# Optimization experiments

Hardware: AMD Instinct MI355X
Metric: run time of the kernel (lower is better)

## Reference

```python
import jax, jax.numpy as jnp
import numpy as np

B, C, CI, H, W = 4, 64, 32, 96, 96  # batch, in_channels, inter_channels, height, width


def conv2d(x, w, b, stride=1, pad=0):
    out = jax.lax.conv_general_dilated(
        x, w, (stride, stride), [(pad, pad), (pad, pad)],
        dimension_numbers=('NCHW', 'OIHW', 'NCHW'))
    return out + b[None, :, None, None]


def maxpool2(x):
    return jax.lax.reduce_window(x, -jnp.inf, jax.lax.max, (1, 1, 2, 2), (1, 1, 2, 2), 'VALID')


def up2(x):
    return jnp.repeat(jnp.repeat(x, 2, axis=2), 2, axis=3)


def bn_train(x, gamma, beta, eps=1e-5):
    # BatchNorm2d in training mode: batch statistics over (N, H, W)
    m = jnp.mean(x, axis=(0, 2, 3), keepdims=True)
    v = jnp.var(x, axis=(0, 2, 3), keepdims=True)
    return gamma[None, :, None, None] * (x - m) * jax.lax.rsqrt(v + eps) + beta[None, :, None, None]


def setup_inputs() -> dict:
    key = jax.random.key(0)
    ks = jax.random.split(key, 20)
    s1 = (2.0 / C) ** 0.5            # kaiming-ish for 1x1 convs
    s3 = (2.0 / (C * 9)) ** 0.5      # kaiming-ish for 3x3 convs
    sw = (2.0 / CI) ** 0.5
    return {
        'x':         jax.random.normal(ks[0], (B, C, H, W), jnp.float32),
        'x_pan':     jax.random.normal(ks[1], (B, C, H, W), jnp.float32),
        'g_w':       jax.random.normal(ks[2], (CI, C, 1, 1), jnp.float32) * s1,
        'g_b':       jnp.zeros((CI,), jnp.float32),
        'g_pan_w':   jax.random.normal(ks[3], (CI, C, 1, 1), jnp.float32) * s1,
        'g_pan_b':   jnp.zeros((CI,), jnp.float32),
        'theta_w':   jax.random.normal(ks[4], (CI, C, 3, 3), jnp.float32) * s3,
        'theta_b':   jax.random.normal(ks[5], (CI,), jnp.float32) * 0.02,
        'phi_w':     jax.random.normal(ks[6], (CI, C, 3, 3), jnp.float32) * s3,
        'phi_b':     jax.random.normal(ks[7], (CI,), jnp.float32) * 0.02,
        'phi_pan_w': jax.random.normal(ks[8], (CI, C, 3, 3), jnp.float32) * s3,
        'phi_pan_b': jax.random.normal(ks[9], (CI,), jnp.float32) * 0.02,
        'W_w':       jax.random.normal(ks[10], (C, CI, 1, 1), jnp.float32) * sw,
        'W_b':       jnp.zeros((C,), jnp.float32),
        'W_gamma':   jnp.ones((C,), jnp.float32),
        'W_beta':    jnp.zeros((C,), jnp.float32),
        'Wp_w':      jax.random.normal(ks[11], (C, CI, 1, 1), jnp.float32) * sw,
        'Wp_b':      jnp.zeros((C,), jnp.float32),
        'Wp_gamma':  jnp.ones((C,), jnp.float32),
        'Wp_beta':   jnp.zeros((C,), jnp.float32),
    }


def reference(x, x_pan, g_w, g_b, g_pan_w, g_pan_b, theta_w, theta_b,
              phi_w, phi_b, phi_pan_w, phi_pan_b,
              W_w, W_b, W_gamma, W_beta, Wp_w, Wp_b, Wp_gamma, Wp_beta):
    b = x.shape[0]
    # self branch
    g_x = maxpool2(conv2d(x, g_w, g_b)).reshape(b, CI, -1)                           # (B,CI,M)
    theta = up2(conv2d(x, theta_w, theta_b, stride=2, pad=1)).reshape(b, CI, -1)     # (B,CI,N)
    phi = up2(maxpool2(conv2d(x, phi_w, phi_b, stride=2, pad=1))).reshape(b, CI, -1) # (B,CI,M)
    f = jnp.einsum('bcn,bcm->bnm', theta, phi)                                       # (B,N,M)
    a = jax.nn.softmax(f, axis=-1)
    y = jnp.einsum('bnm,bcm->bcn', a, g_x).reshape(b, CI, H, W)
    W_y = bn_train(conv2d(y, W_w, W_b), W_gamma, W_beta)
    # cross-modal (pan) branch, sharing theta queries
    g_p = maxpool2(conv2d(x_pan, g_pan_w, g_pan_b)).reshape(b, CI, -1)
    phi_p = up2(maxpool2(conv2d(x_pan, phi_pan_w, phi_pan_b, stride=2, pad=1))).reshape(b, CI, -1)
    f_p = jnp.einsum('bcn,bcm->bnm', theta, phi_p)
    a_p = jax.nn.softmax(f_p, axis=-1)
    y_p = jnp.einsum('bnm,bcm->bcn', a_p, g_p).reshape(b, CI, H, W)
    Wp_y = bn_train(conv2d(y_p, Wp_w, Wp_b), Wp_gamma, Wp_beta)
    return jnp.concatenate([W_y, Wp_y], axis=1)  # (B, 2C, H, W)
```

## Files before the change

kernel.cpp:

```cpp
#include <hip/hip_runtime.h>
#include <math.h>

#define BB   4
#define CIN  64
#define CMID 32
#define HS   96
#define WS   96
#define H2   48
#define W2   48
#define H4   24
#define W4   24
#define N2   (H2*W2)
#define M4   (H4*W4)

__global__ __launch_bounds__(128) void conv3x3_kernel(
    const float* __restrict__ x, const float* __restrict__ x_pan,
    const float* __restrict__ theta_w, const float* __restrict__ phi_w,
    const float* __restrict__ phi_pan_w,
    float* __restrict__ Ptheta, float* __restrict__ Pphi)
{
    const int bx = blockIdx.x;
    const int b  = blockIdx.y;
    const int cz = blockIdx.z;

    __shared__ __align__(16) float xs[8][5][104];
    __shared__ float wsm[8][9][32];

    const int tid = threadIdx.x;
    const int c16 = tid & 15;
    const int g   = tid >> 4;

    const float* xin = (cz == 2) ? x_pan : x;
    const float* wgt = (cz == 0) ? theta_w : (cz == 1 ? phi_w : phi_pan_w);

    const int p    = bx >> 1;
    const int half = bx & 1;
    const int row0 = 4*p - 1;

    float acc[2][2][6];
    #pragma unroll
    for (int u = 0; u < 2; ++u)
        #pragma unroll
        for (int o = 0; o < 2; ++o)
            #pragma unroll
            for (int j = 0; j < 6; ++j) acc[u][o][j] = 0.f;

    for (int chunk = 0; chunk < 4; ++chunk) {
        const int ci0 = half*32 + chunk*8;
        __syncthreads();
        for (int u = tid; u < 8*5*26; u += 128) {
            int ci = u / 130, rem = u % 130, rr = rem / 26, k = rem % 26;
            int row = row0 + rr;
            float4 v = {0.f,0.f,0.f,0.f};
            if (row >= 0 && row < HS && k >= 2)
                v = *(const float4*)&xin[((b*CIN + ci0 + ci)*HS + row)*WS + 4*k - 8];
            *(float4*)&xs[ci][rr][4*k] = v;
        }
        for (int u = tid; u < 576; u += 128) {
            int c2 = u / 18, f = u % 18;
            float4 wv = *(const float4*)&wgt[c2*576 + ci0*9 + 4*f];
            int lin = 4*f;
            wsm[(lin  )/9][(lin  )%9][c2] = wv.x;
            wsm[(lin+1)/9][(lin+1)%9][c2] = wv.y;
            wsm[(lin+2)/9][(lin+2)%9][c2] = wv.z;
            wsm[(lin+3)/9][(lin+3)%9][c2] = wv.w;
        }
        __syncthreads();

        for (int ci = 0; ci < 8; ++ci) {
            float w9a[9], w9b[9];
            #pragma unroll
            for (int kk = 0; kk < 9; ++kk) {
                w9a[kk] = wsm[ci][kk][c16];
                w9b[kk] = wsm[ci][kk][c16 + 16];
            }
            #pragma unroll
            for (int rr = 0; rr < 5; ++rr) {
                const float4* xr = (const float4*)&xs[ci][rr][12*g + 4];
                float4 t0 = xr[0], t1 = xr[1], t2 = xr[2], t3 = xr[3];
                float xv[16] = {t0.x,t0.y,t0.z,t0.w, t1.x,t1.y,t1.z,t1.w,
                                t2.x,t2.y,t2.z,t2.w, t3.x,t3.y,t3.z,t3.w};
                if (rr <= 2) {
                    #pragma unroll
                    for (int j = 0; j < 6; ++j)
                        #pragma unroll
                        for (int kw = 0; kw < 3; ++kw) {
                            float xvv = xv[3 + 2*j + kw];
                            acc[0][0][j] += w9a[rr*3+kw] * xvv;
                            acc[1][0][j] += w9b[rr*3+kw] * xvv;
                        }
                }
                if (rr >= 2) {
                    #pragma unroll
                    for (int j = 0; j < 6; ++j)
                        #pragma unroll
                        for (int kw = 0; kw < 3; ++kw) {
                            float xvv = xv[3 + 2*j + kw];
                            acc[0][1][j] += w9a[(rr-2)*3+kw] * xvv;
                            acc[1][1][j] += w9b[(rr-2)*3+kw] * xvv;
                        }
                }
            }
        }
    }

    if (cz == 0) {
        #pragma unroll
        for (int u = 0; u < 2; ++u)
            #pragma unroll
            for (int o = 0; o < 2; ++o)
                #pragma unroll
                for (int j = 0; j < 6; ++j) {
                    int n = (2*p + o)*48 + 6*g + j;
                    Ptheta[((size_t)(half*4 + b)*N2 + n)*32 + c16 + 16*u] = acc[u][o][j];
                }
    } else {
        const int brn = cz - 1;
        #pragma unroll
        for (int u = 0; u < 2; ++u) {
            float* Pb = Pphi + (size_t)(((half*2 + brn)*4 + b)*32 + c16 + 16*u)*N2;
            #pragma unroll
            for (int o = 0; o < 2; ++o)
                #pragma unroll
                for (int j = 0; j < 6; ++j)
                    Pb[(2*p + o)*48 + 6*g + j] = acc[u][o][j];
        }
    }
}

__global__ __launch_bounds__(256) void phipool_kernel(
    const float* __restrict__ Pphi,
    const float* __restrict__ phi_b, const float* __restrict__ phi_pan_b,
    float* __restrict__ Kp)
{
    const int o = blockIdx.x*256 + threadIdx.x;
    const int br   = o / 73728;
    const int rem  = o % 73728;
    const int b    = rem / 18432;
    const int rem2 = rem % 18432;
    const int co   = rem2 / 576;
    const int k    = rem2 % 576;
    const int pr   = k / 24, pc = k % 24;

    const int h1 = 2*4*32*N2;
    const int base = (((br*4 + b)*32 + co)*48 + 2*pr)*48 + 2*pc;
    float2 a0 = *(const float2*)&Pphi[base];
    float2 a1 = *(const float2*)&Pphi[base + 48];
    float2 c0 = *(const float2*)&Pphi[h1 + base];
    float2 c1 = *(const float2*)&Pphi[h1 + base + 48];
    float v00 = a0.x + c0.x, v01 = a0.y + c0.y;
    float v10 = a1.x + c1.x, v11 = a1.y + c1.y;
    float bv = (br ? phi_pan_b : phi_b)[co];
    Kp[((size_t)(br*4 + b)*576 + k)*32 + co] =
        fmaxf(fmaxf(v00, v01), fmaxf(v10, v11)) + bv;
}

__global__ __launch_bounds__(384) void gconv_kernel(
    const float* __restrict__ x, const float* __restrict__ x_pan,
    const float* __restrict__ g_w, const float* __restrict__ g_b,
    const float* __restrict__ g_pan_w, const float* __restrict__ g_pan_b,
    float* __restrict__ Vt)
{
    const int r4 = blockIdx.x;
    const int ch = blockIdx.y;
    const int bb = blockIdx.z;
    const int br = bb >> 2, b = bb & 3;
    const float* xin = br ? x_pan : x;
    const float* wg  = br ? g_pan_w : g_w;

    __shared__ __align__(16) float xs[32][4][48];
    __shared__ float wl[64*33];
    const int tid = threadIdx.x;
    for (int u = tid; u < 2048; u += 384) {
        int c2 = u >> 6, ci = u & 63;
        wl[ci*33 + c2] = wg[u];
    }

    const int c  = tid & 31;
    const int sl = tid >> 5;
    float4 ac0 = {0,0,0,0}, ac1 = {0,0,0,0}, ac2 = {0,0,0,0}, ac3 = {0,0,0,0};

    for (int ci0 = 0; ci0 < 64; ci0 += 32) {
        __syncthreads();
        for (int u = tid; u < 32*4*12; u += 384) {
            int ci = u / 48, rem = u % 48, r = rem / 12, k = rem % 12;
            *(float4*)&xs[ci][r][4*k] =
                *(const float4*)&xin[((b*64 + ci0 + ci)*96 + 4*r4 + r)*96 + ch*48 + 4*k];
        }
        __syncthreads();
        for (int ci = 0; ci < 32; ++ci) {
            const float wv = wl[(ci0 + ci)*33 + c];
            float4 x0 = *(const float4*)&xs[ci][0][4*sl];
            float4 x1 = *(const float4*)&xs[ci][1][4*sl];
            float4 x2 = *(const float4*)&xs[ci][2][4*sl];
            float4 x3 = *(const float4*)&xs[ci][3][4*sl];
            ac0.x += wv*x0.x; ac0.y += wv*x0.y; ac0.z += wv*x0.z; ac0.w += wv*x0.w;
            ac1.x += wv*x1.x; ac1.y += wv*x1.y; ac1.z += wv*x1.z; ac1.w += wv*x1.w;
            ac2.x += wv*x2.x; ac2.y += wv*x2.y; ac2.z += wv*x2.z; ac2.w += wv*x2.w;
            ac3.x += wv*x3.x; ac3.y += wv*x3.y; ac3.z += wv*x3.z; ac3.w += wv*x3.w;
        }
    }
    float m00 = fmaxf(fmaxf(ac0.x, ac0.y), fmaxf(ac1.x, ac1.y));
    float m01 = fmaxf(fmaxf(ac0.z, ac0.w), fmaxf(ac1.z, ac1.w));
    float m10 = fmaxf(fmaxf(ac2.x, ac2.y), fmaxf(ac3.x, ac3.y));
    float m11 = fmaxf(fmaxf(ac2.z, ac2.w), fmaxf(ac3.z, ac3.w));
    float bv = (br ? g_pan_b : g_b)[c];
    const int k = r4*24 + ch*12 + sl;
    Vt[((size_t)bb*32 + c)*576 + k] = 0.25f*(m00+m01+m10+m11) + bv;
}

__global__ __launch_bounds__(576, 5) void attn_kernel(
    const float* __restrict__ Ptheta, const float* __restrict__ theta_b,
    const float* __restrict__ Kp, const float* __restrict__ Vt,
    const float* __restrict__ W_w, const float* __restrict__ W_b,
    const float* __restrict__ Wp_w, const float* __restrict__ Wp_b,
    float* __restrict__ zbuf, float* __restrict__ Pp1, float* __restrict__ Pp2)
{
    const int qt = blockIdx.x;
    const int bb = blockIdx.y;
    const int b  = bb & 3;
    const int br = bb >> 2;
    const int q0 = qt*16;

    __shared__ __align__(16) float Pt[16*580];
    __shared__ __align__(16) float Qs[16*36];
    __shared__ float ybuf[16*36];
    __shared__ float Wt[32*64];
    __shared__ float zinv[16];
    __shared__ float s1b[512], s2b[512];

    const int tid = threadIdx.x;

    if (tid < 512) {
        const int q = tid >> 5, c = tid & 31;
        Qs[q*36 + c] = Ptheta[((size_t)b*N2 + q0 + q)*32 + c]
                     + Ptheta[((size_t)(4 + b)*N2 + q0 + q)*32 + c]
                     + theta_b[c];
    }
    const float* Wsrc = br ? Wp_w : W_w;
    for (int u = tid; u < 2048; u += 576) {
        const int o = u >> 5, c = u & 31;
        Wt[c*64 + o] = Wsrc[u];
    }
    __syncthreads();

    {
        const float* krow = Kp + ((size_t)bb*576 + tid)*32;
        float4 kf[8];
        #pragma unroll
        for (int i = 0; i < 8; ++i) kf[i] = ((const float4*)krow)[i];
        float s[16];
        #pragma unroll
        for (int q = 0; q < 16; ++q) {
            const float4* qr = (const float4*)&Qs[q*36];
            float a0 = 0.f, a1 = 0.f, a2 = 0.f, a3 = 0.f;
            #pragma unroll
            for (int i = 0; i < 8; ++i) {
                float4 qf = qr[i];
                a0 += qf.x*kf[i].x; a1 += qf.y*kf[i].y;
                a2 += qf.z*kf[i].z; a3 += qf.w*kf[i].w;
            }
            s[q] = (a0 + a1) + (a2 + a3);
        }
        #pragma unroll
        for (int q = 0; q < 16; ++q) Pt[q*580 + tid] = s[q];
    }
    __syncthreads();

    if (tid < 256) {
        const int q = tid >> 4, sl = tid & 15;
        float* row = &Pt[q*580 + 36*sl];
        float4 f[9];
        #pragma unroll
        for (int j = 0; j < 9; ++j) f[j] = *(const float4*)&row[4*j];
        float m = -1e30f;
        #pragma unroll
        for (int j = 0; j < 9; ++j)
            m = fmaxf(m, fmaxf(fmaxf(f[j].x, f[j].y), fmaxf(f[j].z, f[j].w)));
        m = fmaxf(m, __shfl_xor(m, 1));
        m = fmaxf(m, __shfl_xor(m, 2));
        m = fmaxf(m, __shfl_xor(m, 4));
        m = fmaxf(m, __shfl_xor(m, 8));
        float z = 0.f;
        #pragma unroll
        for (int j = 0; j < 9; ++j) {
            f[j].x = __expf(f[j].x - m); f[j].y = __expf(f[j].y - m);
            f[j].z = __expf(f[j].z - m); f[j].w = __expf(f[j].w - m);
            z += (f[j].x + f[j].y) + (f[j].z + f[j].w);
            *(float4*)&row[4*j] = f[j];
        }
        z += __shfl_xor(z, 1); z += __shfl_xor(z, 2);
        z += __shfl_xor(z, 4); z += __shfl_xor(z, 8);
        if (sl == 0) zinv[q] = 1.0f / z;
    }
    __syncthreads();

    if (tid < 512) {
        const int q = tid >> 5, c = tid & 31;
        const float* vrow = Vt + ((size_t)bb*32 + c)*576;
        const float* prow = &Pt[q*580];
        float a0 = 0.f, a1 = 0.f, a2 = 0.f, a3 = 0.f;
        #pragma unroll 4
        for (int kk = 0; kk < 144; ++kk) {
            float4 pa = *(const float4*)&prow[4*kk];
            float4 va = *(const float4*)&vrow[4*kk];
            a0 += pa.x*va.x; a1 += pa.y*va.y;
            a2 += pa.z*va.z; a3 += pa.w*va.w;
        }
        ybuf[q*36 + c] = ((a0 + a1) + (a2 + a3)) * zinv[q];
    }
    __syncthreads();

    if (tid < 512) {
        const int q = tid >> 5, o2 = tid & 31;
        const float* Wbias = br ? Wp_b : W_b;
        float z0a = 0.f, z0b = 0.f, z1a = 0.f, z1b = 0.f;
        #pragma unroll
        for (int c2 = 0; c2 < 32; c2 += 2) {
            float y0 = ybuf[q*36 + c2], y1 = ybuf[q*36 + c2 + 1];
            z0a += Wt[c2*64 + o2]*y0;        z0b += Wt[(c2+1)*64 + o2]*y1;
            z1a += Wt[c2*64 + o2 + 32]*y0;   z1b += Wt[(c2+1)*64 + o2 + 32]*y1;
        }
        float z0 = Wbias[o2]      + z0a + z0b;
        float z1 = Wbias[o2 + 32] + z1a + z1b;
        const int n = q0 + q;
        zbuf[((size_t)(br*64 + o2)*4 + b)*N2 + n]      = z0;
        zbuf[((size_t)(br*64 + o2 + 32)*4 + b)*N2 + n] = z1;
        float t0 = z0 + __shfl_xor(z0, 32);
        float t1 = z1 + __shfl_xor(z1, 32);
        float u0 = z0*z0; u0 += __shfl_xor(u0, 32);
        float u1 = z1*z1; u1 += __shfl_xor(u1, 32);
        if ((tid & 32) == 0) {
            const int w = tid >> 6;
            s1b[w*64 + o2]      = t0;  s1b[w*64 + o2 + 32] = t1;
            s2b[w*64 + o2]      = u0;  s2b[w*64 + o2 + 32] = u1;
        }
    }
    __syncthreads();
    if (tid < 64) {
        float ps = 0.f, pq = 0.f;
        #pragma unroll
        for (int w = 0; w < 8; ++w) { ps += s1b[w*64 + tid]; pq += s2b[w*64 + tid]; }
        Pp1[(size_t)(br*64 + tid)*576 + b*144 + qt] = ps;
        Pp2[(size_t)(br*64 + tid)*576 + b*144 + qt] = pq;
    }
}

__global__ __launch_bounds__(576) void bnup_kernel(
    const float* __restrict__ zbuf,
    const float* __restrict__ Pp1, const float* __restrict__ Pp2,
    const float* __restrict__ W_gamma, const float* __restrict__ W_beta,
    const float* __restrict__ Wp_gamma, const float* __restrict__ Wp_beta,
    float* __restrict__ out)
{
    const int og = blockIdx.x, b = blockIdx.y;
    const int br = og >> 6, o = og & 63;
    const int t = threadIdx.x;

    __shared__ float sb1[9], sb2[9], bc[2];
    float ps = Pp1[(size_t)og*576 + t];
    float pq = Pp2[(size_t)og*576 + t];
    #pragma unroll
    for (int d = 1; d < 64; d <<= 1) {
        ps += __shfl_xor(ps, d);
        pq += __shfl_xor(pq, d);
    }
    if ((t & 63) == 0) { sb1[t >> 6] = ps; sb2[t >> 6] = pq; }
    __syncthreads();
    if (t == 0) {
        float s = 0.f, qq = 0.f;
        #pragma unroll
        for (int w = 0; w < 9; ++w) { s += sb1[w]; qq += sb2[w]; }
        const float mean = s * (1.0f/9216.0f);
        const float var  = qq * (1.0f/9216.0f) - mean*mean;
        const float gamma = (br ? Wp_gamma : W_gamma)[o];
        const float beta  = (br ? Wp_beta  : W_beta)[o];
        const float scale = gamma * rsqrtf(var + 1e-5f);
        bc[0] = scale; bc[1] = beta - mean*scale;
    }
    __syncthreads();
    const float scale = bc[0], shift = bc[1];

    float4 a = *(const float4*)&zbuf[((size_t)og*4 + b)*N2 + 4*t];
    const int r = t / 12, cs = t % 12;
    float v0 = a.x*scale + shift, v1 = a.y*scale + shift;
    float v2 = a.z*scale + shift, v3 = a.w*scale + shift;
    float4 lo = {v0, v0, v1, v1};
    float4 hi = {v2, v2, v3, v3};
    float* ob = out + ((size_t)(b*128 + og)*96 + 2*r)*96 + 8*cs;
    *(float4*)(ob)       = lo;
    *(float4*)(ob + 4)   = hi;
    *(float4*)(ob + 96)  = lo;
    *(float4*)(ob + 100) = hi;
}

extern "C" void kernel_launch(void* const* d_in, const int* in_sizes, int n_in,
                              void* d_out, int out_size, void* d_ws, size_t ws_size,
                              hipStream_t stream) {
    (void)in_sizes; (void)n_in; (void)out_size; (void)ws_size;
    const float* x         = (const float*)d_in[0];
    const float* x_pan     = (const float*)d_in[1];
    const float* g_w       = (const float*)d_in[2];
    const float* g_b       = (const float*)d_in[3];
    const float* g_pan_w   = (const float*)d_in[4];
    const float* g_pan_b   = (const float*)d_in[5];
    const float* theta_w   = (const float*)d_in[6];
    const float* theta_b   = (const float*)d_in[7];
    const float* phi_w     = (const float*)d_in[8];
    const float* phi_b     = (const float*)d_in[9];
    const float* phi_pan_w = (const float*)d_in[10];
    const float* phi_pan_b = (const float*)d_in[11];
    const float* W_w       = (const float*)d_in[12];
    const float* W_b       = (const float*)d_in[13];
    const float* W_gamma   = (const float*)d_in[14];
    const float* W_beta    = (const float*)d_in[15];
    const float* Wp_w      = (const float*)d_in[16];
    const float* Wp_b      = (const float*)d_in[17];
    const float* Wp_gamma  = (const float*)d_in[18];
    const float* Wp_beta   = (const float*)d_in[19];

    float* out = (float*)d_out;
    float* ws  = (float*)d_ws;

    float* Ptheta = ws;
    float* Pphi   = Ptheta + 589824;
    float* zbuf   = Pphi;
    float* Kp     = Pphi + 1179648;
    float* Vt     = Kp + 147456;
    float* Pp1    = Vt + 147456;
    float* Pp2    = Pp1 + 73728;

    conv3x3_kernel<<<dim3(48, 4, 3), 128, 0, stream>>>(
        x, x_pan, theta_w, phi_w, phi_pan_w, Ptheta, Pphi);
    phipool_kernel<<<dim3(576), 256, 0, stream>>>(Pphi, phi_b, phi_pan_b, Kp);
    gconv_kernel<<<dim3(24, 2, 8), 384, 0, stream>>>(
        x, x_pan, g_w, g_b, g_pan_w, g_pan_b, Vt);
    attn_kernel<<<dim3(144, 8), 576, 0, stream>>>(
        Ptheta, theta_b, Kp, Vt, W_w, W_b, Wp_w, Wp_b, zbuf, Pp1, Pp2);
    bnup_kernel<<<dim3(128, 4), 576, 0, stream>>>(
        zbuf, Pp1, Pp2, W_gamma, W_beta, Wp_gamma, Wp_beta, out);
}
```

Baseline: 444.6 us.

## Split conv3x3 output rows across more threads and stage V tiles in shared memory

The 3x3 conv kernel doubles its block to 256 threads. Each thread half now computes one output row instead of two, and each staging chunk loads 16 input channels instead of 8. The attention kernel drops the occupancy hint from its launch bounds, pads the score rows differently, and stages Vt in 144-column chunks in shared memory for the P·V product instead of streaming it from global memory per thread. The goals are more parallelism in the conv and coalesced, reused V loads in attention, at the cost of more shared memory and extra barriers.

```diff
diff --git a/kernel.cpp b/kernel.cpp
--- a/kernel.cpp
+++ b/kernel.cpp
@@ -13,7 +13,7 @@
 #define N2   (H2*W2)
 #define M4   (H4*W4)
 
-__global__ __launch_bounds__(128) void conv3x3_kernel(
+__global__ __launch_bounds__(256) void conv3x3_kernel(
     const float* __restrict__ x, const float* __restrict__ x_pan,
     const float* __restrict__ theta_w, const float* __restrict__ phi_w,
     const float* __restrict__ phi_pan_w,
@@ -23,12 +23,13 @@
     const int b  = blockIdx.y;
     const int cz = blockIdx.z;
 
-    __shared__ __align__(16) float xs[8][5][104];
-    __shared__ float wsm[8][9][32];
+    __shared__ __align__(16) float xs[16][5][104];
+    __shared__ float wsm[16][9][32];
 
     const int tid = threadIdx.x;
     const int c16 = tid & 15;
-    const int g   = tid >> 4;
+    const int g   = (tid >> 4) & 7;
+    const int r   = tid >> 7;
 
     const float* xin = (cz == 2) ? x_pan : x;
     const float* wgt = (cz == 0) ? theta_w : (cz == 1 ? phi_w : phi_pan_w);
@@ -37,18 +38,16 @@
     const int half = bx & 1;
     const int row0 = 4*p - 1;
 
-    float acc[2][2][6];
+    float acc[2][6];
     #pragma unroll
     for (int u = 0; u < 2; ++u)
         #pragma unroll
-        for (int o = 0; o < 2; ++o)
-            #pragma unroll
-            for (int j = 0; j < 6; ++j) acc[u][o][j] = 0.f;
-
-    for (int chunk = 0; chunk < 4; ++chunk) {
-        const int ci0 = half*32 + chunk*8;
-        __syncthreads();
-        for (int u = tid; u < 8*5*26; u += 128) {
+        for (int j = 0; j < 6; ++j) acc[u][j] = 0.f;
+
+    for (int chunk = 0; chunk < 2; ++chunk) {
+        const int ci0 = half*32 + chunk*16;
+        __syncthreads();
+        for (int u = tid; u < 16*5*26; u += 256) {
             int ci = u / 130, rem = u % 130, rr = rem / 26, k = rem % 26;
             int row = row0 + rr;
             float4 v = {0.f,0.f,0.f,0.f};
@@ -56,8 +55,8 @@
                 v = *(const float4*)&xin[((b*CIN + ci0 + ci)*HS + row)*WS + 4*k - 8];
             *(float4*)&xs[ci][rr][4*k] = v;
         }
-        for (int u = tid; u < 576; u += 128) {
-            int c2 = u / 18, f = u % 18;
+        for (int u = tid; u < 1152; u += 256) {
+            int c2 = u / 36, f = u % 36;
             float4 wv = *(const float4*)&wgt[c2*576 + ci0*9 + 4*f];
             int lin = 4*f;
             wsm[(lin  )/9][(lin  )%9][c2] = wv.x;
@@ -67,7 +66,7 @@
         }
         __syncthreads();
 
-        for (int ci = 0; ci < 8; ++ci) {
+        for (int ci = 0; ci < 16; ++ci) {
             float w9a[9], w9b[9];
             #pragma unroll
             for (int kk = 0; kk < 9; ++kk) {
@@ -75,55 +74,38 @@
                 w9b[kk] = wsm[ci][kk][c16 + 16];
             }
             #pragma unroll
-            for (int rr = 0; rr < 5; ++rr) {
-                const float4* xr = (const float4*)&xs[ci][rr][12*g + 4];
+            for (int rr2 = 0; rr2 < 3; ++rr2) {
+                const float4* xr = (const float4*)&xs[ci][2*r + rr2][12*g + 4];
                 float4 t0 = xr[0], t1 = xr[1], t2 = xr[2], t3 = xr[3];
                 float xv[16] = {t0.x,t0.y,t0.z,t0.w, t1.x,t1.y,t1.z,t1.w,
                                 t2.x,t2.y,t2.z,t2.w, t3.x,t3.y,t3.z,t3.w};
-                if (rr <= 2) {
+                #pragma unroll
+                for (int j = 0; j < 6; ++j)
                     #pragma unroll
-                    for (int j = 0; j < 6; ++j)
-                        #pragma unroll
-                        for (int kw = 0; kw < 3; ++kw) {
-                            float xvv = xv[3 + 2*j + kw];
-                            acc[0][0][j] += w9a[rr*3+kw] * xvv;
-                            acc[1][0][j] += w9b[rr*3+kw] * xvv;
-                        }
-                }
-                if (rr >= 2) {
-                    #pragma unroll
-                    for (int j = 0; j < 6; ++j)
-                        #pragma unroll
-                        for (int kw = 0; kw < 3; ++kw) {
-                            float xvv = xv[3 + 2*j + kw];
-                            acc[0][1][j] += w9a[(rr-2)*3+kw] * xvv;
-                            acc[1][1][j] += w9b[(rr-2)*3+kw] * xvv;
-                        }
-                }
+                    for (int kw = 0; kw < 3; ++kw) {
+                        float xvv = xv[3 + 2*j + kw];
+                        acc[0][j] += w9a[rr2*3+kw] * xvv;
+                        acc[1][j] += w9b[rr2*3+kw] * xvv;
+                    }
             }
         }
     }
 
+    const int n0 = (2*p + r)*48 + 6*g;
     if (cz == 0) {
         #pragma unroll
         for (int u = 0; u < 2; ++u)
             #pragma unroll
-            for (int o = 0; o < 2; ++o)
-                #pragma unroll
-                for (int j = 0; j < 6; ++j) {
-                    int n = (2*p + o)*48 + 6*g + j;
-                    Ptheta[((size_t)(half*4 + b)*N2 + n)*32 + c16 + 16*u] = acc[u][o][j];
-                }
+            for (int j = 0; j < 6; ++j)
+                Ptheta[((size_t)(half*4 + b)*N2 + n0 + j)*32 + c16 + 16*u] = acc[u][j];
     } else {
         const int brn = cz - 1;
         #pragma unroll
         for (int u = 0; u < 2; ++u) {
             float* Pb = Pphi + (size_t)(((half*2 + brn)*4 + b)*32 + c16 + 16*u)*N2;
             #pragma unroll
-            for (int o = 0; o < 2; ++o)
-                #pragma unroll
-                for (int j = 0; j < 6; ++j)
-                    Pb[(2*p + o)*48 + 6*g + j] = acc[u][o][j];
+            for (int j = 0; j < 6; ++j)
+                Pb[n0 + j] = acc[u][j];
         }
     }
 }
@@ -209,7 +191,7 @@
     Vt[((size_t)bb*32 + c)*576 + k] = 0.25f*(m00+m01+m10+m11) + bv;
 }
 
-__global__ __launch_bounds__(576, 5) void attn_kernel(
+__global__ __launch_bounds__(576) void attn_kernel(
     const float* __restrict__ Ptheta, const float* __restrict__ theta_b,
     const float* __restrict__ Kp, const float* __restrict__ Vt,
     const float* __restrict__ W_w, const float* __restrict__ W_b,
@@ -222,10 +204,12 @@
     const int br = bb >> 2;
     const int q0 = qt*16;
 
-    __shared__ __align__(16) float Pt[16*580];
     __shared__ __align__(16) float Qs[16*36];
+    __shared__ __align__(16) float Pt[16*577];
+    __shared__ __align__(16) float Vc[32*145];
+    __shared__ float Wt[32*64];
+    __shared__ float Wbia[64];
     __shared__ float ybuf[16*36];
-    __shared__ float Wt[32*64];
     __shared__ float zinv[16];
     __shared__ float s1b[512], s2b[512];
 
@@ -238,18 +222,16 @@
                      + theta_b[c];
     }
     const float* Wsrc = br ? Wp_w : W_w;
-    for (int u = tid; u < 2048; u += 576) {
-        const int o = u >> 5, c = u & 31;
-        Wt[c*64 + o] = Wsrc[u];
-    }
+    for (int u = tid; u < 2048; u += 576)
+        Wt[(u & 31)*64 + (u >> 5)] = Wsrc[u];
+    if (tid < 64) Wbia[tid] = (br ? Wp_b : W_b)[tid];
     __syncthreads();
 
     {
-        const float* krow = Kp + ((size_t)bb*576 + tid)*32;
+        const float4* krow = (const float4*)(Kp + ((size_t)bb*576 + tid)*32);
         float4 kf[8];
         #pragma unroll
-        for (int i = 0; i < 8; ++i) kf[i] = ((const float4*)krow)[i];
-        float s[16];
+        for (int i = 0; i < 8; ++i) kf[i] = krow[i];
         #pragma unroll
         for (int q = 0; q < 16; ++q) {
             const float4* qr = (const float4*)&Qs[q*36];
@@ -260,16 +242,14 @@
                 a0 += qf.x*kf[i].x; a1 += qf.y*kf[i].y;
                 a2 += qf.z*kf[i].z; a3 += qf.w*kf[i].w;
             }
-            s[q] = (a0 + a1) + (a2 + a3);
-        }
-        #pragma unroll
-        for (int q = 0; q < 16; ++q) Pt[q*580 + tid] = s[q];
+            Pt[q*577 + tid] = (a0 + a1) + (a2 + a3);
+        }
     }
     __syncthreads();
 
     if (tid < 256) {
         const int q = tid >> 4, sl = tid & 15;
-        float* row = &Pt[q*580 + 36*sl];
+        float* row = &Pt[q*577 + 36*sl];
         float4 f[9];
         #pragma unroll
         for (int j = 0; j < 9; ++j) f[j] = *(const float4*)&row[4*j];
@@ -295,34 +275,46 @@
     }
     __syncthreads();
 
+    const int q2 = tid >> 5, c2i = tid & 31;
+    float a0 = 0.f, a1 = 0.f, a2 = 0.f, a3 = 0.f;
+    for (int ch = 0; ch < 4; ++ch) {
+        const int k0 = ch*144;
+        #pragma unroll
+        for (int i = 0; i < 2; ++i) {
+            const int u = tid + 576*i;
+            const int c = u / 36, kq = u % 36;
+            *(float4*)&Vc[c*145 + 4*kq] =
+                *(const float4*)&Vt[((size_t)bb*32 + c)*576 + k0 + 4*kq];
+        }
+        __syncthreads();
+        if (tid < 512) {
+            const float* prow = &Pt[q2*577 + k0];
+            const float* vrow = &Vc[c2i*145];
+            #pragma unroll 6
+            for (int kk = 0; kk < 36; ++kk) {
+                float4 pa = *(const float4*)&prow[4*kk];
+                float4 va = *(const float4*)&vrow[4*kk];
+                a0 += pa.x*va.x; a1 += pa.y*va.y;
+                a2 += pa.z*va.z; a3 += pa.w*va.w;
+            }
+        }
+        __syncthreads();
+    }
+    if (tid < 512)
+        ybuf[q2*36 + c2i] = ((a0 + a1) + (a2 + a3)) * zinv[q2];
+    __syncthreads();
+
     if (tid < 512) {
-        const int q = tid >> 5, c = tid & 31;
-        const float* vrow = Vt + ((size_t)bb*32 + c)*576;
-        const float* prow = &Pt[q*580];
-        float a0 = 0.f, a1 = 0.f, a2 = 0.f, a3 = 0.f;
-        #pragma unroll 4
-        for (int kk = 0; kk < 144; ++kk) {
-            float4 pa = *(const float4*)&prow[4*kk];
-            float4 va = *(const float4*)&vrow[4*kk];
-            a0 += pa.x*va.x; a1 += pa.y*va.y;
-            a2 += pa.z*va.z; a3 += pa.w*va.w;
-        }
-        ybuf[q*36 + c] = ((a0 + a1) + (a2 + a3)) * zinv[q];
-    }
-    __syncthreads();
-
-    if (tid < 512) {
-        const int q = tid >> 5, o2 = tid & 31;
-        const float* Wbias = br ? Wp_b : W_b;
+        const int q = q2, o2 = c2i;
         float z0a = 0.f, z0b = 0.f, z1a = 0.f, z1b = 0.f;
         #pragma unroll
-        for (int c2 = 0; c2 < 32; c2 += 2) {
-            float y0 = ybuf[q*36 + c2], y1 = ybuf[q*36 + c2 + 1];
-            z0a += Wt[c2*64 + o2]*y0;        z0b += Wt[(c2+1)*64 + o2]*y1;
-            z1a += Wt[c2*64 + o2 + 32]*y0;   z1b += Wt[(c2+1)*64 + o2 + 32]*y1;
-        }
-        float z0 = Wbias[o2]      + z0a + z0b;
-        float z1 = Wbias[o2 + 32] + z1a + z1b;
+        for (int c = 0; c < 32; c += 2) {
+            float y0 = ybuf[q*36 + c], y1 = ybuf[q*36 + c + 1];
+            z0a += Wt[c*64 + o2]*y0;        z0b += Wt[(c+1)*64 + o2]*y1;
+            z1a += Wt[c*64 + o2 + 32]*y0;   z1b += Wt[(c+1)*64 + o2 + 32]*y1;
+        }
+        float z0 = Wbia[o2]      + z0a + z0b;
+        float z1 = Wbia[o2 + 32] + z1a + z1b;
         const int n = q0 + q;
         zbuf[((size_t)(br*64 + o2)*4 + b)*N2 + n]      = z0;
         zbuf[((size_t)(br*64 + o2 + 32)*4 + b)*N2 + n] = z1;
@@ -430,7 +422,7 @@
     float* Pp1    = Vt + 147456;
     float* Pp2    = Pp1 + 73728;
 
-    conv3x3_kernel<<<dim3(48, 4, 3), 128, 0, stream>>>(
+    conv3x3_kernel<<<dim3(48, 4, 3), 256, 0, stream>>>(
         x, x_pan, theta_w, phi_w, phi_pan_w, Ptheta, Pphi);
     phipool_kernel<<<dim3(576), 256, 0, stream>>>(Pphi, phi_b, phi_pan_b, Kp);
     gconv_kernel<<<dim3(24, 2, 8), 384, 0, stream>>>(
```

Measured after the change: 576.2 us. +29.6%, slower.
